# Performance work log

Measured on AMD Instinct MI355X. Metric: run time of the kernel, lower is better.

Reference implementation:

```python
import jax, jax.numpy as jnp
import numpy as np

B, N, T, D, H, E = 2, 1024, 8, 128, 4, 8192
DH = D // H
NEG_SLOPE = 0.2  # GATv2Conv default negative_slope


def _ln(x, g, b):
    m = jnp.mean(x, -1, keepdims=True)
    v = jnp.mean((x - m) ** 2, -1, keepdims=True)
    return (x - m) * jax.lax.rsqrt(v + 1e-5) * g + b


def _forward(x, edge_index, gat_wl, gat_wr, gat_att, gat_b, in_w, in_b, out_w, out_b,
             ffn_w1, ffn_b1, ffn_w2, ffn_b2, fus_w, fus_b,
             lns_g, lns_b, lnt1_g, lnt1_b, lnt2_g, lnt2_b, lnf_g, lnf_b):
    # ---- spatial branch: GATv2, vectorized over (B, T) instead of python loops ----
    loops = jnp.arange(N)
    src = jnp.concatenate([edge_index[0], loops])  # j: message source (PyG adds self loops)
    dst = jnp.concatenate([edge_index[1], loops])  # i: aggregation target
    xl = jnp.einsum('bntd,de->bnte', x, gat_wl).reshape(B, N, T, H, D)
    xr = jnp.einsum('bntd,de->bnte', x, gat_wr).reshape(B, N, T, H, D)
    ml = xl[:, src]                                  # [B,Et,T,H,D]
    mr = xr[:, dst]
    e = jax.nn.leaky_relu(ml + mr, NEG_SLOPE)
    logits = jnp.einsum('bethd,hd->beth', e, gat_att)
    logits = jnp.moveaxis(logits, 1, 0)              # [Et,B,T,H]
    mx = jax.ops.segment_max(logits, dst, num_segments=N)
    p = jnp.exp(logits - mx[dst])                    # stable edge softmax per dst node
    ssum = jax.ops.segment_sum(p, dst, num_segments=N)
    alpha = p / ssum[dst]                            # [Et,B,T,H]
    msg = alpha[..., None] * jnp.moveaxis(ml, 1, 0)
    agg = jax.ops.segment_sum(msg, dst, num_segments=N)  # [N,B,T,H,D]
    x_sp = jnp.moveaxis(agg.mean(3), 0, 1) + gat_b   # concat=False -> head mean; [B,N,T,D]
    x_sp = _ln(x_sp, lns_g, lns_b)

    # ---- temporal branch: MHA + FFN, vectorized over all B*N nodes ----
    xt = x.reshape(B * N, T, D)
    qkv = xt @ in_w + in_b
    q, k, v = jnp.split(qkv, 3, axis=-1)
    q = q.reshape(B * N, T, H, DH)
    k = k.reshape(B * N, T, H, DH)
    v = v.reshape(B * N, T, H, DH)
    scores = jnp.einsum('bthd,bshd->bhts', q, k) / np.float32(np.sqrt(DH))
    attn = jax.nn.softmax(scores, -1)
    o = jnp.einsum('bhts,bshd->bthd', attn, v).reshape(B * N, T, D)
    o = o @ out_w + out_b
    x1 = _ln(xt + o, lnt1_g, lnt1_b)
    ffn = jax.nn.gelu(x1 @ ffn_w1 + ffn_b1, approximate=False) @ ffn_w2 + ffn_b2
    x_tp = _ln(x1 + ffn, lnt2_g, lnt2_b).reshape(B, N, T, D)

    # ---- gated fusion with residual ----
    g = jax.nn.sigmoid(jnp.concatenate([x_sp, x_tp], -1) @ fus_w + fus_b)
    return _ln(g * x_sp + (1.0 - g) * x_tp + x, lnf_g, lnf_b)


def setup_inputs() -> dict:
    key = jax.random.key(0)
    ks = jax.random.split(key, 12)
    s = 0.05
    f = jnp.float32
    return {
        'x': jax.random.normal(ks[0], (B, N, T, D), f),
        'edge_index': jax.random.randint(ks[1], (2, E), 0, N),
        'gat_wl': jax.random.normal(ks[2], (D, H * D), f) * s,
        'gat_wr': jax.random.normal(ks[3], (D, H * D), f) * s,
        'gat_att': jax.random.normal(ks[4], (H, D), f) * s,
        'gat_b': jnp.zeros((D,), f),
        'in_w': jax.random.normal(ks[5], (D, 3 * D), f) * s,
        'in_b': jnp.zeros((3 * D,), f),
        'out_w': jax.random.normal(ks[6], (D, D), f) * s,
        'out_b': jnp.zeros((D,), f),
        'ffn_w1': jax.random.normal(ks[7], (D, 4 * D), f) * s,
        'ffn_b1': jnp.zeros((4 * D,), f),
        'ffn_w2': jax.random.normal(ks[8], (4 * D, D), f) * s,
        'ffn_b2': jnp.zeros((D,), f),
        'fus_w': jax.random.normal(ks[9], (2 * D, D), f) * s,
        'fus_b': jnp.zeros((D,), f),
        'lns_g': jnp.ones((D,), f), 'lns_b': jnp.zeros((D,), f),
        'lnt1_g': jnp.ones((D,), f), 'lnt1_b': jnp.zeros((D,), f),
        'lnt2_g': jnp.ones((D,), f), 'lnt2_b': jnp.zeros((D,), f),
        'lnf_g': jnp.ones((D,), f), 'lnf_b': jnp.zeros((D,), f),
    }


def reference(x, edge_index, gat_wl, gat_wr, gat_att, gat_b, in_w, in_b, out_w, out_b,
              ffn_w1, ffn_b1, ffn_w2, ffn_b2, fus_w, fus_b,
              lns_g, lns_b, lnt1_g, lnt1_b, lnt2_g, lnt2_b, lnf_g, lnf_b):
    return _forward(x, edge_index, gat_wl, gat_wr, gat_att, gat_b, in_w, in_b, out_w, out_b,
                    ffn_w1, ffn_b1, ffn_w2, ffn_b2, fus_w, fus_b,
                    lns_g, lns_b, lnt1_g, lnt1_b, lnt2_g, lnt2_b, lnf_g, lnf_b)
```

## Files before the change

### kernel.cpp

```cpp
#include <hip/hip_runtime.h>
#include <math.h>

#define B_ 2
#define N_ 1024
#define T_ 8
#define D_ 128
#define H_ 4
#define E_ 8192
#define EN_ 9216
#define M_ 16384

typedef unsigned short u16;
using bf16x8 = __attribute__((ext_vector_type(8))) short;
using f32x4  = __attribute__((ext_vector_type(4))) float;

__device__ __forceinline__ float bf2f(unsigned int u) {
  return __uint_as_float(u << 16);
}
__device__ __forceinline__ u16 f2bf(float f) {
  unsigned int x = __float_as_uint(f);
  x += 0x7fffu + ((x >> 16) & 1u);
  return (u16)(x >> 16);
}
__device__ __forceinline__ void load8f(const u16* p, float* f) {
  uint4 u = *(const uint4*)p;
  f[0]=bf2f(u.x & 0xffffu); f[1]=bf2f(u.x >> 16);
  f[2]=bf2f(u.y & 0xffffu); f[3]=bf2f(u.y >> 16);
  f[4]=bf2f(u.z & 0xffffu); f[5]=bf2f(u.z >> 16);
  f[6]=bf2f(u.w & 0xffffu); f[7]=bf2f(u.w >> 16);
}
__device__ __forceinline__ void unpack8(uint4 u, float* f) {
  f[0]=bf2f(u.x & 0xffffu); f[1]=bf2f(u.x >> 16);
  f[2]=bf2f(u.y & 0xffffu); f[3]=bf2f(u.y >> 16);
  f[4]=bf2f(u.z & 0xffffu); f[5]=bf2f(u.z >> 16);
  f[6]=bf2f(u.w & 0xffffu); f[7]=bf2f(u.w >> 16);
}
__device__ __forceinline__ void gl2lds(const u16* g, u16* l) {
  __builtin_amdgcn_global_load_lds(
      (const __attribute__((address_space(1))) unsigned int*)(const void*)g,
      (__attribute__((address_space(3))) unsigned int*)(void*)l,
      16, 0, 0);
}

__device__ __forceinline__ u16 conv_w_elem(int idx,
    const float* wl, const float* wr, const float* inw, const float* outw,
    const float* f1, const float* f2, const float* fw) {
  const float* src; int base, K, N;
  if      (idx < 65536)  { src = wl;   base = 0;      K = 128; N = 512; }
  else if (idx < 131072) { src = wr;   base = 65536;  K = 128; N = 512; }
  else if (idx < 180224) { src = inw;  base = 131072; K = 128; N = 384; }
  else if (idx < 196608) { src = outw; base = 180224; K = 128; N = 128; }
  else if (idx < 262144) { src = f1;   base = 196608; K = 128; N = 512; }
  else if (idx < 327680) { src = f2;   base = 262144; K = 512; N = 128; }
  else                   { src = fw;   base = 327680; K = 256; N = 128; }
  int o = idx - base;
  int n = o / K, k = o - n * K;
  return f2bf(src[k * N + n]);
}

__global__ __launch_bounds__(1024) void prep_csr_k(const float* __restrict__ x,
    const float* __restrict__ wl, const float* __restrict__ wr,
    const float* __restrict__ inw, const float* __restrict__ outw,
    const float* __restrict__ f1, const float* __restrict__ f2,
    const float* __restrict__ fw,
    u16* __restrict__ XB, u16* __restrict__ WB,
    const int* __restrict__ ei, int* __restrict__ offs, int* __restrict__ srcs) {
  __shared__ int cnt[N_];
  __shared__ int cur[N_];
  int bi = blockIdx.x;
  int tid = threadIdx.x;
  if (bi < 512) {
    int i = (bi * 1024 + tid) * 4;
    float4 v = *(const float4*)&x[i];
    u16 o[4] = {f2bf(v.x), f2bf(v.y), f2bf(v.z), f2bf(v.w)};
    *(ushort4*)&XB[i] = *(ushort4*)o;
    return;
  }
  if (bi < 600) {
    int base = (bi - 512) * 4096 + tid * 4;
#pragma unroll
    for (int j = 0; j < 4; ++j)
      WB[base + j] = conv_w_elem(base + j, wl, wr, inw, outw, f1, f2, fw);
    return;
  }
  cnt[tid] = 0;
  __syncthreads();
  for (int e = tid; e < EN_; e += 1024) {
    int d = (e < E_) ? ei[E_ + e] : (e - E_);
    atomicAdd(&cnt[d], 1);
  }
  __syncthreads();
  int mine = cnt[tid];
  for (int off = 1; off < 1024; off <<= 1) {
    int tv = (tid >= off) ? cnt[tid - off] : 0;
    __syncthreads();
    cnt[tid] += tv;
    __syncthreads();
  }
  int excl = cnt[tid] - mine;
  offs[tid] = excl;
  if (tid == 1023) offs[N_] = cnt[1023];
  cur[tid] = excl;
  __syncthreads();
  for (int e = tid; e < EN_; e += 1024) {
    int d = (e < E_) ? ei[E_ + e] : (e - E_);
    int s = (e < E_) ? ei[e] : (e - E_);
    int pos = atomicAdd(&cur[d], 1);
    srcs[pos] = s;
  }
}

template<int BM, int ACT, int ROUTE>
__device__ __forceinline__ void gemm_tile(int bx, int by,
    const u16* A, int lda, const u16* WT, int K, const float* bias,
    u16* C, int ldc, u16* R0, u16* R1, u16* R2, const float* b2,
    u16* As, u16* Bs) {
  constexpr int MI = BM / 32;
  int tid = threadIdx.x;
  int lane = tid & 63, wid = tid >> 6;
  int lr = lane & 15, lk = lane >> 4;
  int wm = (wid >> 1) * (BM / 2);
  int wn = (wid & 1) * 64;

  u16* Cb; int ldc_; int col0; const float* bias_;
  if (ROUTE) {
    if (bx < 4)      { Cb = R0; ldc_ = 512; col0 = bx * 128;       bias_ = nullptr; }
    else if (bx < 8) { Cb = R1; ldc_ = 512; col0 = (bx - 4) * 128; bias_ = nullptr; }
    else             { Cb = R2; ldc_ = 384; col0 = (bx - 8) * 128; bias_ = b2; }
  } else { Cb = C; ldc_ = ldc; col0 = bx * 128; bias_ = bias; }

  f32x4 acc[MI][4] = {};
  for (int k0 = 0; k0 < K; k0 += 32) {
    __syncthreads();
#pragma unroll
    for (int i = 0; i < BM / 64; ++i) {
      int o = tid * 16 + i * 4096;
      int row = o >> 6;
      int col = (o >> 1) & 31;
      gl2lds(A + (size_t)(by * BM + row) * lda + k0 + col,
             (u16*)((char*)As + wid * 1024 + i * 4096));
    }
#pragma unroll
    for (int i = 0; i < 2; ++i) {
      int o = tid * 16 + i * 4096;
      int nrow = o >> 6;
      int col = (o >> 1) & 31;
      gl2lds(WT + (size_t)(bx * 128 + nrow) * K + k0 + col,
             (u16*)((char*)Bs + wid * 1024 + i * 4096));
    }
    __syncthreads();
    bf16x8 bf[4];
#pragma unroll
    for (int ni = 0; ni < 4; ++ni)
      bf[ni] = *(const bf16x8*)&Bs[(wn + ni * 16 + lr) * 32 + lk * 8];
#pragma unroll
    for (int mi = 0; mi < MI; ++mi) {
      bf16x8 af = *(const bf16x8*)&As[(wm + mi * 16 + lr) * 32 + lk * 8];
#pragma unroll
      for (int ni = 0; ni < 4; ++ni)
        acc[mi][ni] = __builtin_amdgcn_mfma_f32_16x16x32_bf16(af, bf[ni], acc[mi][ni], 0, 0, 0);
    }
  }
  float bc[4];
#pragma unroll
  for (int ni = 0; ni < 4; ++ni)
    bc[ni] = bias_ ? bias_[col0 + wn + ni * 16 + lr] : 0.f;
#pragma unroll
  for (int mi = 0; mi < MI; ++mi) {
#pragma unroll
    for (int r = 0; r < 4; ++r) {
      int row = by * BM + wm + mi * 16 + lk * 4 + r;
#pragma unroll
      for (int ni = 0; ni < 4; ++ni) {
        int col = col0 + wn + ni * 16 + lr;
        float v = acc[mi][ni][r] + bc[ni];
        if (ACT) v = 0.5f * v * (1.f + erff(v * 0.70710678118f));
        Cb[(size_t)row * ldc_ + col] = f2bf(v);
      }
    }
  }
}

template<int EPI>
__device__ __forceinline__ void ln_epilogue(int by, f32x4 (&acc)[2][4],
    const float* bias, const float* xres, const u16* xcat,
    const float* lng, const float* lnb,
    float* o32, u16* o16, int os16, float* rs, float* rq) {
  int tid = threadIdx.x;
  int lane = tid & 63, wid = tid >> 6;
  int lr = lane & 15, lk = lane >> 4;
  int wm = (wid >> 1) * 32, wn = (wid & 1) * 64;
  float bc[4];
#pragma unroll
  for (int ni = 0; ni < 4; ++ni) bc[ni] = bias[wn + ni * 16 + lr];
#pragma unroll
  for (int mi = 0; mi < 2; ++mi) {
#pragma unroll
    for (int r = 0; r < 4; ++r) {
      int row = by * 64 + wm + mi * 16 + lk * 4 + r;
      float s = 0.f, s2 = 0.f;
#pragma unroll
      for (int ni = 0; ni < 4; ++ni) {
        int col = wn + ni * 16 + lr;
        float v = acc[mi][ni][r] + bc[ni];
        if (EPI == 1 || EPI == 2) {
          v += xres[(size_t)row * 128 + col];
        } else {
          float gg = 1.f / (1.f + __expf(-v));
          float xsp = bf2f(xcat[(size_t)row * 256 + col]);
          float xtp = bf2f(xcat[(size_t)row * 256 + 128 + col]);
          v = gg * xsp + (1.f - gg) * xtp + xres[(size_t)row * 128 + col];
        }
        acc[mi][ni][r] = v;
        s += v; s2 += v * v;
      }
      s += __shfl_xor(s, 1, 64); s2 += __shfl_xor(s2, 1, 64);
      s += __shfl_xor(s, 2, 64); s2 += __shfl_xor(s2, 2, 64);
      s += __shfl_xor(s, 4, 64); s2 += __shfl_xor(s2, 4, 64);
      s += __shfl_xor(s, 8, 64); s2 += __shfl_xor(s2, 8, 64);
      if (lr == 0) {
        int rl = wm + mi * 16 + lk * 4 + r;
        rs[rl * 2 + (wid & 1)] = s;
        rq[rl * 2 + (wid & 1)] = s2;
      }
    }
  }
  __syncthreads();
#pragma unroll
  for (int mi = 0; mi < 2; ++mi) {
#pragma unroll
    for (int r = 0; r < 4; ++r) {
      int rl = wm + mi * 16 + lk * 4 + r;
      int row = by * 64 + rl;
      float tot = rs[rl * 2] + rs[rl * 2 + 1];
      float tq = rq[rl * 2] + rq[rl * 2 + 1];
      float mean = tot * (1.f / 128.f);
      float var = tq * (1.f / 128.f) - mean * mean;
      float rinv = rsqrtf(var + 1e-5f);
#pragma unroll
      for (int ni = 0; ni < 4; ++ni) {
        int col = wn + ni * 16 + lr;
        float o = (acc[mi][ni][r] - mean) * rinv * lng[col] + lnb[col];
        if (EPI != 2) o32[(size_t)row * 128 + col] = o;
        if (EPI != 3) o16[(size_t)row * os16 + col] = f2bf(o);
      }
    }
  }
}

__global__ __launch_bounds__(256) void fusion_k(const u16* __restrict__ A,
    const u16* __restrict__ WT, const float* __restrict__ bias,
    const float* __restrict__ xres, const u16* __restrict__ xcat,
    const float* __restrict__ lng, const float* __restrict__ lnb,
    float* __restrict__ o32) {
  __shared__ u16 As[64 * 32];
  __shared__ u16 Bs[128 * 32];
  __shared__ float rs[128], rq[128];
  int by = blockIdx.x;
  int tid = threadIdx.x;
  int lane = tid & 63, wid = tid >> 6;
  int lr = lane & 15, lk = lane >> 4;
  int wm = (wid >> 1) * 32, wn = (wid & 1) * 64;
  const int K = 256;

  f32x4 acc[2][4] = {};
  for (int k0 = 0; k0 < K; k0 += 32) {
    __syncthreads();
    {
      int o = tid * 16;
      int row = o >> 6;
      int col = (o >> 1) & 31;
      gl2lds(A + (size_t)(by * 64 + row) * K + k0 + col,
             (u16*)((char*)As + wid * 1024));
    }
#pragma unroll
    for (int i = 0; i < 2; ++i) {
      int o = tid * 16 + i * 4096;
      int nrow = o >> 6;
      int col = (o >> 1) & 31;
      gl2lds(WT + (size_t)nrow * K + k0 + col,
             (u16*)((char*)Bs + wid * 1024 + i * 4096));
    }
    __syncthreads();
    bf16x8 bf[4];
#pragma unroll
    for (int ni = 0; ni < 4; ++ni)
      bf[ni] = *(const bf16x8*)&Bs[(wn + ni * 16 + lr) * 32 + lk * 8];
#pragma unroll
    for (int mi = 0; mi < 2; ++mi) {
      bf16x8 af = *(const bf16x8*)&As[(wm + mi * 16 + lr) * 32 + lk * 8];
#pragma unroll
      for (int ni = 0; ni < 4; ++ni)
        acc[mi][ni] = __builtin_amdgcn_mfma_f32_16x16x32_bf16(af, bf[ni], acc[mi][ni], 0, 0, 0);
    }
  }
  ln_epilogue<3>(by, acc, bias, xres, xcat, lng, lnb, o32, nullptr, 0, rs, rq);
}

__global__ __launch_bounds__(256) void proj_k(const u16* __restrict__ XB,
    const u16* __restrict__ WT1, const float* __restrict__ in_b,
    u16* __restrict__ XL, u16* __restrict__ XR, u16* __restrict__ QKV) {
  __shared__ u16 As[128 * 32];
  __shared__ u16 Bs[128 * 32];
  gemm_tile<128, 0, 1>(blockIdx.x, blockIdx.y, XB, 128, WT1, 128, nullptr,
                       nullptr, 0, XL, XR, QKV, in_b, As, Bs);
}

__device__ __forceinline__ void gat_wave(int w, int lane,
    const u16* XL, const u16* XR, const int* offs, const int* srcs,
    const float* att, const float* gb, const float* lng, const float* lnb,
    u16* XCAT) {
  int n = w >> 4;
  int b = (w >> 3) & 1;
  int t = w & 7;
  int dd = (lane & 15) * 8;
  size_t tokn = (size_t)(b * N_ + n) * 8 + t;
  size_t rowoff = (size_t)b * (N_ * 8) + t;

  float mr[8], av[8];
  load8f(XR + tokn * 512 + lane * 8, mr);
  *(float4*)&av[0] = *(const float4*)(att + lane * 8);
  *(float4*)&av[4] = *(const float4*)(att + lane * 8 + 4);

  int beg = offs[n], end = offs[n + 1];
  float sH = 0.f;
  float acc[8] = {0.f, 0.f, 0.f, 0.f, 0.f, 0.f, 0.f, 0.f};
  int i = beg;
  uint4 r0 = *(const uint4*)(XL + (rowoff + (size_t)srcs[i] * 8) * 512 + lane * 8);
  uint4 r1 = r0;
  if (i + 1 < end)
    r1 = *(const uint4*)(XL + (rowoff + (size_t)srcs[i + 1] * 8) * 512 + lane * 8);
  while (i + 1 < end) {
    uint4 c0 = r0, c1 = r1;
    if (i + 2 < end)
      r0 = *(const uint4*)(XL + (rowoff + (size_t)srcs[i + 2] * 8) * 512 + lane * 8);
    if (i + 3 < end)
      r1 = *(const uint4*)(XL + (rowoff + (size_t)srcs[i + 3] * 8) * 512 + lane * 8);
    float ml0[8], ml1[8];
    unpack8(c0, ml0);
    unpack8(c1, ml1);
    float d0 = 0.f, d1 = 0.f;
#pragma unroll
    for (int j = 0; j < 8; ++j) {
      float m0 = ml0[j] + mr[j];
      m0 = fmaxf(m0, 0.2f * m0);
      d0 += m0 * av[j];
      float m1 = ml1[j] + mr[j];
      m1 = fmaxf(m1, 0.2f * m1);
      d1 += m1 * av[j];
    }
    d0 += __shfl_xor(d0, 1, 64); d1 += __shfl_xor(d1, 1, 64);
    d0 += __shfl_xor(d0, 2, 64); d1 += __shfl_xor(d1, 2, 64);
    d0 += __shfl_xor(d0, 4, 64); d1 += __shfl_xor(d1, 4, 64);
    d0 += __shfl_xor(d0, 8, 64); d1 += __shfl_xor(d1, 8, 64);
    float p0 = __expf(d0), p1 = __expf(d1);
    sH += p0 + p1;
#pragma unroll
    for (int j = 0; j < 8; ++j) acc[j] += p0 * ml0[j] + p1 * ml1[j];
    i += 2;
  }
  if (i < end) {
    float ml0[8];
    unpack8(r0, ml0);
    float d0 = 0.f;
#pragma unroll
    for (int j = 0; j < 8; ++j) {
      float m0 = ml0[j] + mr[j];
      m0 = fmaxf(m0, 0.2f * m0);
      d0 += m0 * av[j];
    }
    d0 += __shfl_xor(d0, 1, 64);
    d0 += __shfl_xor(d0, 2, 64);
    d0 += __shfl_xor(d0, 4, 64);
    d0 += __shfl_xor(d0, 8, 64);
    float p0 = __expf(d0);
    sH += p0;
#pragma unroll
    for (int j = 0; j < 8; ++j) acc[j] += p0 * ml0[j];
  }
  float invS = 1.f / sH;
#pragma unroll
  for (int j = 0; j < 8; ++j) acc[j] *= invS;
#pragma unroll
  for (int j = 0; j < 8; ++j) {
    acc[j] += __shfl_xor(acc[j], 16, 64);
    acc[j] += __shfl_xor(acc[j], 32, 64);
  }
#pragma unroll
  for (int j = 0; j < 8; ++j) acc[j] = acc[j] * 0.25f + gb[dd + j];
  float s = 0.f, s2 = 0.f;
#pragma unroll
  for (int j = 0; j < 8; ++j) { s += acc[j]; s2 += acc[j] * acc[j]; }
#pragma unroll
  for (int m = 1; m < 16; m <<= 1) {
    s += __shfl_xor(s, m, 64);
    s2 += __shfl_xor(s2, m, 64);
  }
  float mean = s * (1.f / 128.f);
  float var = s2 * (1.f / 128.f) - mean * mean;
  float r = rsqrtf(var + 1e-5f);
  if (lane < 16) {
    u16 ob[8];
#pragma unroll
    for (int j = 0; j < 8; ++j)
      ob[j] = f2bf((acc[j] - mean) * r * lng[dd + j] + lnb[dd + j]);
    *(uint4*)&XCAT[tokn * 256 + dd] = *(uint4*)ob;
  }
}

__global__ __launch_bounds__(256) void attn_gat_k(const u16* __restrict__ QKV,
    const u16* __restrict__ WTO, const float* __restrict__ out_b,
    const float* __restrict__ x,
    const float* __restrict__ lnt1_g, const float* __restrict__ lnt1_b,
    float* __restrict__ X1, u16* __restrict__ X1B,
    const u16* __restrict__ XL, const u16* __restrict__ XR,
    const int* __restrict__ offs, const int* __restrict__ srcs,
    const float* __restrict__ att, const float* __restrict__ gb,
    const float* __restrict__ lns_g, const float* __restrict__ lns_b,
    u16* __restrict__ XCAT) {
  __shared__ u16 As[4 * 64 * 32];
  __shared__ u16 Bs[2 * 128 * 32];
  __shared__ float rs[128], rq[128];
  int bid = blockIdx.x;
  int tid = threadIdx.x;
  int lane = tid & 63, wid = tid >> 6;

  if (bid >= 256) {
    gat_wave((bid - 256) * 4 + wid, lane, XL, XR, offs, srcs,
             att, gb, lns_g, lns_b, XCAT);
    return;
  }
  int by = bid;
  {
    int o = tid * 16;
    gl2lds(WTO + (size_t)(o >> 6) * 128 + ((o >> 1) & 31),
           (u16*)((char*)Bs + wid * 1024));
    o = tid * 16 + 4096;
    gl2lds(WTO + (size_t)(o >> 6) * 128 + ((o >> 1) & 31),
           (u16*)((char*)Bs + 4096 + wid * 1024));
  }
  int t = lane >> 3, sidx = lane & 7, dg = lane & 7;
  for (int it = 0; it < 8; ++it) {
    int task = wid * 8 + it;
    int bnl = task >> 2, h = task & 3;
    int bn = by * 8 + bnl;
    const u16* base = QKV + (size_t)bn * 8 * 384;
    float va[8][4];
#pragma unroll
    for (int s2 = 0; s2 < 8; ++s2) {
      ushort4 vv = *(const ushort4*)(base + s2 * 384 + 256 + h * 32 + dg * 4);
      va[s2][0] = bf2f(vv.x); va[s2][1] = bf2f(vv.y);
      va[s2][2] = bf2f(vv.z); va[s2][3] = bf2f(vv.w);
    }
    const u16* qp = base + t * 384 + h * 32;
    const u16* kp = base + sidx * 384 + 128 + h * 32;
    float sc = 0.f;
#pragma unroll
    for (int d0 = 0; d0 < 32; d0 += 8) {
      float q[8], k[8];
      load8f(qp + d0, q);
      load8f(kp + d0, k);
#pragma unroll
      for (int j = 0; j < 8; ++j) sc += q[j] * k[j];
    }
    sc *= 0.17677669529663687f;
    float m = sc;
    m = fmaxf(m, __shfl_xor(m, 1, 64));
    m = fmaxf(m, __shfl_xor(m, 2, 64));
    m = fmaxf(m, __shfl_xor(m, 4, 64));
    float p = __expf(sc - m);
    float S = p;
    S += __shfl_xor(S, 1, 64);
    S += __shfl_xor(S, 2, 64);
    S += __shfl_xor(S, 4, 64);
    float alpha = p / S;
    int tb = lane & 56;
    float o0 = 0.f, o1 = 0.f, o2 = 0.f, o3 = 0.f;
#pragma unroll
    for (int s2 = 0; s2 < 8; ++s2) {
      float a = __shfl(alpha, tb + s2, 64);
      o0 += a * va[s2][0];
      o1 += a * va[s2][1];
      o2 += a * va[s2][2];
      o3 += a * va[s2][3];
    }
    u16 ov[4] = {f2bf(o0), f2bf(o1), f2bf(o2), f2bf(o3)};
    int row = bnl * 8 + t;
    *(ushort4*)&As[h * 2048 + row * 32 + dg * 4] = *(ushort4*)ov;
  }
  int lr = lane & 15, lk = lane >> 4;
  int wm = (wid >> 1) * 32, wn = (wid & 1) * 64;
  f32x4 acc[2][4] = {};
  for (int kc = 0; kc < 4; ++kc) {
    __syncthreads();
    if (kc < 3) {
      char* dstb = (char*)Bs + ((kc + 1) & 1) * 8192;
      int o = tid * 16;
      gl2lds(WTO + (size_t)(o >> 6) * 128 + (kc + 1) * 32 + ((o >> 1) & 31),
             (u16*)(dstb + wid * 1024));
      o = tid * 16 + 4096;
      gl2lds(WTO + (size_t)(o >> 6) * 128 + (kc + 1) * 32 + ((o >> 1) & 31),
             (u16*)(dstb + 4096 + wid * 1024));
    }
    const u16* Bc = Bs + (kc & 1) * 4096;
    bf16x8 bf[4];
#pragma unroll
    for (int ni = 0; ni < 4; ++ni)
      bf[ni] = *(const bf16x8*)&Bc[(wn + ni * 16 + lr) * 32 + lk * 8];
#pragma unroll
    for (int mi = 0; mi < 2; ++mi) {
      bf16x8 af = *(const bf16x8*)&As[kc * 2048 + (wm + mi * 16 + lr) * 32 + lk * 8];
#pragma unroll
      for (int ni = 0; ni < 4; ++ni)
        acc[mi][ni] = __builtin_amdgcn_mfma_f32_16x16x32_bf16(af, bf[ni], acc[mi][ni], 0, 0, 0);
    }
  }
  __syncthreads();
  ln_epilogue<1>(by, acc, out_b, x, nullptr, lnt1_g, lnt1_b, X1, X1B, 128, rs, rq);
}

__global__ __launch_bounds__(256) void ffn_fused_k(const u16* __restrict__ X1B,
    const u16* __restrict__ WTF1, const u16* __restrict__ WTF2,
    const float* __restrict__ b1, const float* __restrict__ b2,
    const float* __restrict__ X1,
    const float* __restrict__ lng, const float* __restrict__ lnb,
    u16* __restrict__ XCATr) {
  __shared__ u16 As[64 * 128];
  __shared__ u16 B1s[64 * 128];
  __shared__ u16 B2s[128 * 64];
  __shared__ u16 Hc[2 * 64 * 40];
  __shared__ float rs[128], rq[128];
  int by = blockIdx.x;
  int tid = threadIdx.x;
  int lane = tid & 63, wid = tid >> 6;
  int lr = lane & 15, lk = lane >> 4;

#pragma unroll
  for (int kc = 0; kc < 4; ++kc) {
    gl2lds(X1B + (size_t)(by * 64 + (tid >> 2)) * 128 + kc * 32 + (tid & 3) * 8,
           (u16*)((char*)As + kc * 4096 + wid * 1024));
  }
  int wr0 = (wid >> 1) * 32, wc0 = (wid & 1) * 32;
  int wm = (wid >> 1) * 32, wn = (wid & 1) * 64;
  f32x4 acc2[2][4] = {};
  for (int nc = 0; nc < 8; ++nc) {
    __syncthreads();
#pragma unroll
    for (int kc = 0; kc < 4; ++kc) {
      gl2lds(WTF1 + (size_t)(nc * 64 + (tid >> 2)) * 128 + kc * 32 + (tid & 3) * 8,
             (u16*)((char*)B1s + kc * 4096 + wid * 1024));
    }
#pragma unroll
    for (int i = 0; i < 4; ++i) {
      int o = tid * 16 + i * 4096;
      int kc2l = o >> 13;
      int wb = o & 8191;
      int nrow = wb >> 6;
      int kin = (wb & 63) >> 1;
      gl2lds(WTF2 + (size_t)nrow * 512 + nc * 64 + kc2l * 32 + kin,
             (u16*)((char*)B2s + wid * 1024 + i * 4096));
    }
    __syncthreads();
    f32x4 a1[2][2] = {};
#pragma unroll
    for (int kc = 0; kc < 4; ++kc) {
      bf16x8 bf0 = *(const bf16x8*)&B1s[kc * 2048 + (wc0 + lr) * 32 + lk * 8];
      bf16x8 bf1 = *(const bf16x8*)&B1s[kc * 2048 + (wc0 + 16 + lr) * 32 + lk * 8];
#pragma unroll
      for (int mi = 0; mi < 2; ++mi) {
        bf16x8 af = *(const bf16x8*)&As[kc * 2048 + (wr0 + mi * 16 + lr) * 32 + lk * 8];
        a1[mi][0] = __builtin_amdgcn_mfma_f32_16x16x32_bf16(af, bf0, a1[mi][0], 0, 0, 0);
        a1[mi][1] = __builtin_amdgcn_mfma_f32_16x16x32_bf16(af, bf1, a1[mi][1], 0, 0, 0);
      }
    }
#pragma unroll
    for (int mi = 0; mi < 2; ++mi) {
#pragma unroll
      for (int r = 0; r < 4; ++r) {
        int row = wr0 + mi * 16 + lk * 4 + r;
#pragma unroll
        for (int ni = 0; ni < 2; ++ni) {
          int cl = wc0 + ni * 16 + lr;
          float v = a1[mi][ni][r] + b1[nc * 64 + cl];
          v = 0.5f * v * (1.f + erff(v * 0.70710678118f));
          Hc[(cl >> 5) * 2560 + row * 40 + (cl & 31)] = f2bf(v);
        }
      }
    }
    __syncthreads();
#pragma unroll
    for (int kc2l = 0; kc2l < 2; ++kc2l) {
      bf16x8 bf[4];
#pragma unroll
      for (int ni = 0; ni < 4; ++ni)
        bf[ni] = *(const bf16x8*)&B2s[kc2l * 4096 + (wn + ni * 16 + lr) * 32 + lk * 8];
#pragma unroll
      for (int mi = 0; mi < 2; ++mi) {
        bf16x8 af = *(const bf16x8*)&Hc[kc2l * 2560 + (wm + mi * 16 + lr) * 40 + lk * 8];
#pragma unroll
        for (int ni = 0; ni < 4; ++ni)
          acc2[mi][ni] = __builtin_amdgcn_mfma_f32_16x16x32_bf16(af, bf[ni], acc2[mi][ni], 0, 0, 0);
      }
    }
  }
  __syncthreads();
  ln_epilogue<2>(by, acc2, b2, X1, nullptr, lng, lnb, nullptr, XCATr, 256, rs, rq);
}

extern "C" void kernel_launch(void* const* d_in, const int* in_sizes, int n_in,
                              void* d_out, int out_size, void* d_ws, size_t ws_size,
                              hipStream_t stream) {
  const float* x       = (const float*)d_in[0];
  const int*   ei      = (const int*)d_in[1];
  const float* gat_att = (const float*)d_in[4];
  const float* gat_b   = (const float*)d_in[5];
  const float* in_b    = (const float*)d_in[7];
  const float* out_b   = (const float*)d_in[9];
  const float* ffn_b1  = (const float*)d_in[11];
  const float* ffn_b2  = (const float*)d_in[13];
  const float* fus_b   = (const float*)d_in[15];
  const float* lns_g   = (const float*)d_in[16];
  const float* lns_b   = (const float*)d_in[17];
  const float* lnt1_g  = (const float*)d_in[18];
  const float* lnt1_b  = (const float*)d_in[19];
  const float* lnt2_g  = (const float*)d_in[20];
  const float* lnt2_b  = (const float*)d_in[21];
  const float* lnf_g   = (const float*)d_in[22];
  const float* lnf_b   = (const float*)d_in[23];

  char* ws = (char*)d_ws;
  u16*   WB    = (u16*)ws;
  u16*   WTO   = WB + 180224;
  u16*   WTF1  = WB + 196608;
  u16*   WTF2  = WB + 262144;
  u16*   WTFUS = WB + 327680;
  int*   OFFS  = (int*)(ws + 3145728);
  int*   SRCS  = (int*)(ws + 3153920);
  u16*   XB   = (u16*)(ws + 4194304);
  u16*   XL   = (u16*)(ws + 8388608);
  u16*   XR   = (u16*)(ws + 25165824);
  float* X1   = (float*)(ws + 41943040);
  u16*   QKV  = (u16*)(ws + 50331648);
  u16*   X1B  = (u16*)(ws + 62914560);
  u16*   XCAT = (u16*)(ws + 67108864);

  prep_csr_k<<<dim3(601), dim3(1024), 0, stream>>>(x,
      (const float*)d_in[2], (const float*)d_in[3], (const float*)d_in[6],
      (const float*)d_in[8], (const float*)d_in[10], (const float*)d_in[12],
      (const float*)d_in[14], XB, WB, ei, OFFS, SRCS);

  proj_k<<<dim3(11, 128), dim3(256), 0, stream>>>(XB, WB, in_b, XL, XR, QKV);

  attn_gat_k<<<dim3(4352), dim3(256), 0, stream>>>(QKV, WTO, out_b, x,
      lnt1_g, lnt1_b, X1, X1B, XL, XR, OFFS, SRCS,
      gat_att, gat_b, lns_g, lns_b, XCAT);

  ffn_fused_k<<<dim3(256), dim3(256), 0, stream>>>(X1B, WTF1, WTF2,
      ffn_b1, ffn_b2, X1, lnt2_g, lnt2_b, XCAT + 128);

  fusion_k<<<dim3(256), dim3(256), 0, stream>>>(XCAT, WTFUS, fus_b, x, XCAT,
      lnf_g, lnf_b, (float*)d_out);
}
```

Measured before the change: 232.3 us.

## Split fused GAT/attention kernel into separate launches and preload full out-proj weight

The combined attn_gat_k kernel, which sent blocks to either GAT aggregation or temporal attention plus output projection, is split into two kernels, gat_k and attn_oproj_k, launched back to back. The attention kernel now loads the whole 128x128 out-proj weight into LDS up front, replacing a double-buffered per-chunk load with per-iteration barriers. This removes divergent block roles and the extra syncs, letting each kernel get its own register/LDS allocation. The cost is an extra launch, the loss of overlap between the two branches, and more LDS per attention block.

```diff
diff --git a/kernel.cpp b/kernel.cpp
--- a/kernel.cpp
+++ b/kernel.cpp
@@ -268,17 +268,13 @@
     __syncthreads();
     {
       int o = tid * 16;
-      int row = o >> 6;
-      int col = (o >> 1) & 31;
-      gl2lds(A + (size_t)(by * 64 + row) * K + k0 + col,
+      gl2lds(A + (size_t)(by * 64 + (o >> 6)) * K + k0 + ((o >> 1) & 31),
              (u16*)((char*)As + wid * 1024));
     }
 #pragma unroll
     for (int i = 0; i < 2; ++i) {
       int o = tid * 16 + i * 4096;
-      int nrow = o >> 6;
-      int col = (o >> 1) & 31;
-      gl2lds(WT + (size_t)nrow * K + k0 + col,
+      gl2lds(WT + (size_t)(o >> 6) * K + k0 + ((o >> 1) & 31),
              (u16*)((char*)Bs + wid * 1024 + i * 4096));
     }
     __syncthreads();
@@ -306,10 +302,14 @@
                        nullptr, 0, XL, XR, QKV, in_b, As, Bs);
 }
 
-__device__ __forceinline__ void gat_wave(int w, int lane,
-    const u16* XL, const u16* XR, const int* offs, const int* srcs,
-    const float* att, const float* gb, const float* lng, const float* lnb,
-    u16* XCAT) {
+__global__ __launch_bounds__(256) void gat_k(const u16* __restrict__ XL,
+    const u16* __restrict__ XR,
+    const int* __restrict__ offs, const int* __restrict__ srcs,
+    const float* __restrict__ att, const float* __restrict__ gb,
+    const float* __restrict__ lng, const float* __restrict__ lnb,
+    u16* __restrict__ XCAT) {
+  int w = blockIdx.x * 4 + (threadIdx.x >> 6);
+  int lane = threadIdx.x & 63;
   int n = w >> 4;
   int b = (w >> 3) & 1;
   int t = w & 7;
@@ -408,37 +408,29 @@
   }
 }
 
-__global__ __launch_bounds__(256) void attn_gat_k(const u16* __restrict__ QKV,
+__global__ __launch_bounds__(256) void attn_oproj_k(const u16* __restrict__ QKV,
     const u16* __restrict__ WTO, const float* __restrict__ out_b,
     const float* __restrict__ x,
     const float* __restrict__ lnt1_g, const float* __restrict__ lnt1_b,
-    float* __restrict__ X1, u16* __restrict__ X1B,
-    const u16* __restrict__ XL, const u16* __restrict__ XR,
-    const int* __restrict__ offs, const int* __restrict__ srcs,
-    const float* __restrict__ att, const float* __restrict__ gb,
-    const float* __restrict__ lns_g, const float* __restrict__ lns_b,
-    u16* __restrict__ XCAT) {
+    float* __restrict__ X1, u16* __restrict__ X1B) {
   __shared__ u16 As[4 * 64 * 32];
-  __shared__ u16 Bs[2 * 128 * 32];
+  __shared__ u16 Bs[4 * 128 * 32];
   __shared__ float rs[128], rq[128];
-  int bid = blockIdx.x;
+  int by = blockIdx.x;
   int tid = threadIdx.x;
   int lane = tid & 63, wid = tid >> 6;
 
-  if (bid >= 256) {
-    gat_wave((bid - 256) * 4 + wid, lane, XL, XR, offs, srcs,
-             att, gb, lns_g, lns_b, XCAT);
-    return;
-  }
-  int by = bid;
-  {
-    int o = tid * 16;
-    gl2lds(WTO + (size_t)(o >> 6) * 128 + ((o >> 1) & 31),
-           (u16*)((char*)Bs + wid * 1024));
-    o = tid * 16 + 4096;
-    gl2lds(WTO + (size_t)(o >> 6) * 128 + ((o >> 1) & 31),
-           (u16*)((char*)Bs + 4096 + wid * 1024));
-  }
+#pragma unroll
+  for (int i = 0; i < 8; ++i) {
+    int o = tid * 16 + i * 4096;
+    int c = o >> 13;
+    int wb = o & 8191;
+    int nrow = wb >> 6;
+    int kin = (wb & 63) >> 1;
+    gl2lds(WTO + (size_t)nrow * 128 + c * 32 + kin,
+           (u16*)((char*)Bs + wid * 1024 + i * 4096));
+  }
+
   int t = lane >> 3, sidx = lane & 7, dg = lane & 7;
   for (int it = 0; it < 8; ++it) {
     int task = wid * 8 + it;
@@ -488,34 +480,25 @@
     int row = bnl * 8 + t;
     *(ushort4*)&As[h * 2048 + row * 32 + dg * 4] = *(ushort4*)ov;
   }
+  __syncthreads();
+
   int lr = lane & 15, lk = lane >> 4;
   int wm = (wid >> 1) * 32, wn = (wid & 1) * 64;
   f32x4 acc[2][4] = {};
-  for (int kc = 0; kc < 4; ++kc) {
-    __syncthreads();
-    if (kc < 3) {
-      char* dstb = (char*)Bs + ((kc + 1) & 1) * 8192;
-      int o = tid * 16;
-      gl2lds(WTO + (size_t)(o >> 6) * 128 + (kc + 1) * 32 + ((o >> 1) & 31),
-             (u16*)(dstb + wid * 1024));
-      o = tid * 16 + 4096;
-      gl2lds(WTO + (size_t)(o >> 6) * 128 + (kc + 1) * 32 + ((o >> 1) & 31),
-             (u16*)(dstb + 4096 + wid * 1024));
-    }
-    const u16* Bc = Bs + (kc & 1) * 4096;
+#pragma unroll
+  for (int c = 0; c < 4; ++c) {
     bf16x8 bf[4];
 #pragma unroll
     for (int ni = 0; ni < 4; ++ni)
-      bf[ni] = *(const bf16x8*)&Bc[(wn + ni * 16 + lr) * 32 + lk * 8];
+      bf[ni] = *(const bf16x8*)&Bs[c * 4096 + (wn + ni * 16 + lr) * 32 + lk * 8];
 #pragma unroll
     for (int mi = 0; mi < 2; ++mi) {
-      bf16x8 af = *(const bf16x8*)&As[kc * 2048 + (wm + mi * 16 + lr) * 32 + lk * 8];
+      bf16x8 af = *(const bf16x8*)&As[c * 2048 + (wm + mi * 16 + lr) * 32 + lk * 8];
 #pragma unroll
       for (int ni = 0; ni < 4; ++ni)
         acc[mi][ni] = __builtin_amdgcn_mfma_f32_16x16x32_bf16(af, bf[ni], acc[mi][ni], 0, 0, 0);
     }
   }
-  __syncthreads();
   ln_epilogue<1>(by, acc, out_b, x, nullptr, lnt1_g, lnt1_b, X1, X1B, 128, rs, rq);
 }
 
@@ -651,9 +634,11 @@
 
   proj_k<<<dim3(11, 128), dim3(256), 0, stream>>>(XB, WB, in_b, XL, XR, QKV);
 
-  attn_gat_k<<<dim3(4352), dim3(256), 0, stream>>>(QKV, WTO, out_b, x,
-      lnt1_g, lnt1_b, X1, X1B, XL, XR, OFFS, SRCS,
+  gat_k<<<dim3(4096), dim3(256), 0, stream>>>(XL, XR, OFFS, SRCS,
       gat_att, gat_b, lns_g, lns_b, XCAT);
+
+  attn_oproj_k<<<dim3(256), dim3(256), 0, stream>>>(QKV, WTO, out_b, x,
+      lnt1_g, lnt1_b, X1, X1B);
 
   ffn_fused_k<<<dim3(256), dim3(256), 0, stream>>>(X1B, WTF1, WTF2,
       ffn_b1, ffn_b2, X1, lnt2_g, lnt2_b, XCAT + 128);
```

Measured after the change: 221.2 us. -4.8%, faster.
